# Optimization experiments

Measured on AMD Instinct MI355X. Metric: run time of the kernel, lower is better.

The kernel has to match this reference:

```python
import jax, jax.numpy as jnp
import numpy as np

NUM_HEAD = 8
HIDDEN = 1024


def setup_inputs() -> dict:
    key = jax.random.key(0)
    ks = jax.random.split(key, 7)
    B, Q, K = 2, 256, 256
    return {
        "query": jax.random.normal(ks[0], (B, Q, HIDDEN), jnp.float32),
        "keys": jax.random.normal(ks[1], (B, K, HIDDEN), jnp.float32),
        "values": jax.random.normal(ks[2], (B, K, HIDDEN), jnp.float32),
        "mask": jax.random.randint(ks[3], (B, K), 0, 2, jnp.int32),
        "W_q": jax.random.normal(ks[4], (HIDDEN, HIDDEN), jnp.float32),
        "W_k": jax.random.normal(ks[5], (HIDDEN, HIDDEN), jnp.float32),
        "V_a": jax.random.normal(ks[6], (HIDDEN,), jnp.float32),
    }


def reference(query, keys, values, mask, W_q, W_k, V_a):
    B, Q, H = query.shape
    K = keys.shape[1]
    h_q = query @ W_q                                   # [B,Q,H]
    h_k = keys @ W_k                                    # [B,K,H]
    # additive (Bahdanau) scores, split hidden into heads and sum per head
    h = jnp.tanh(h_q[:, :, None, :] + h_k[:, None, :, :]) * V_a   # [B,Q,K,H]
    logits = h.reshape(B, Q, K, NUM_HEAD, H // NUM_HEAD).sum(-1)  # [B,Q,K,h]
    logits = jnp.transpose(logits, (0, 3, 1, 2))        # [B,h,Q,K]
    penalty = (1.0 - mask.astype(jnp.float32)) * 99.0   # [B,K]
    logits = logits - penalty[:, None, None, :]
    weights = jax.nn.softmax(logits, axis=-1)           # [B,h,Q,K]
    v = values.reshape(B, K, NUM_HEAD, H // NUM_HEAD)   # [B,K,h,d]
    ctx = jnp.einsum('bhqk,bkhd->bqhd', weights, v).reshape(B, Q, H)
    return ctx, weights
```

## Files before the change

### kernel.cpp

```cpp
#include <hip/hip_runtime.h>
#include <hip/hip_bf16.h>


#define TANH_SCALE 2.88539008177792681472f
#define LOG2E      1.44269504088896340736f

typedef __attribute__((ext_vector_type(8))) short bf16x8_t;
typedef __attribute__((ext_vector_type(4))) float f32x4_t;

__device__ inline ushort bf16_rne(float f) {
  unsigned u = __float_as_uint(f);
  u += 0x7FFFu + ((u >> 16) & 1u);
  return (ushort)(u >> 16);
}
__device__ inline float bf16_to_f(ushort h) { return __uint_as_float((unsigned)h << 16); }
__device__ inline void split1(float v, ushort& hi, ushort& lo) {
  hi = bf16_rne(v);
  lo = bf16_rne(v - bf16_to_f(hi));
}

__global__ __launch_bounds__(256) void prep(
    const float* __restrict__ query, const float* __restrict__ keys,
    const float* __restrict__ Wq, const float* __restrict__ Wk,
    ushort* __restrict__ qhi, ushort* __restrict__ qlo,
    ushort* __restrict__ khi, ushort* __restrict__ klo,
    ushort* __restrict__ wqthi, ushort* __restrict__ wqtlo,
    ushort* __restrict__ wkthi, ushort* __restrict__ wktlo)
{
  __shared__ float t[64][65];
  const int bid = blockIdx.x, tid = threadIdx.x;
  if (bid < 1024) {
    const int z = bid >> 9;
    const float* in = z ? keys : query;
    ushort* hi = z ? khi : qhi;
    ushort* lo = z ? klo : qlo;
    const size_t i = ((size_t)(bid & 511) * 256 + tid) * 4;
    float4 v = *(const float4*)(in + i);
    ushort h0, h1, h2, h3, l0, l1, l2, l3;
    split1(v.x, h0, l0); split1(v.y, h1, l1);
    split1(v.z, h2, l2); split1(v.w, h3, l3);
    *(ushort4*)(hi + i) = make_ushort4(h0, h1, h2, h3);
    *(ushort4*)(lo + i) = make_ushort4(l0, l1, l2, l3);
  } else {
    const int idx = bid - 1024;
    const int z = idx >> 8;
    const float* W = z ? Wk : Wq;
    ushort* thi = z ? wkthi : wqthi;
    ushort* tlo = z ? wktlo : wqtlo;
    const int n0 = (idx & 15) * 64, h0 = ((idx >> 4) & 15) * 64;
    const int r = tid >> 4, c = (tid & 15) * 4;
#pragma unroll
    for (int i = 0; i < 4; ++i) {
      const int rr = r + i * 16;
      float4 wv = *(const float4*)(W + (size_t)(h0 + rr) * 1024 + n0 + c);
      t[rr][c + 0] = wv.x; t[rr][c + 1] = wv.y;
      t[rr][c + 2] = wv.z; t[rr][c + 3] = wv.w;
    }
    __syncthreads();
#pragma unroll
    for (int i = 0; i < 4; ++i) {
      const int rr = r + i * 16;
      ushort h0v, h1v, h2v, h3v, l0v, l1v, l2v, l3v;
      split1(t[c + 0][rr] * TANH_SCALE, h0v, l0v);
      split1(t[c + 1][rr] * TANH_SCALE, h1v, l1v);
      split1(t[c + 2][rr] * TANH_SCALE, h2v, l2v);
      split1(t[c + 3][rr] * TANH_SCALE, h3v, l3v);
      *(ushort4*)(thi + (size_t)(n0 + rr) * 1024 + h0 + c) = make_ushort4(h0v, h1v, h2v, h3v);
      *(ushort4*)(tlo + (size_t)(n0 + rr) * 1024 + h0 + c) = make_ushort4(l0v, l1v, l2v, l3v);
    }
  }
}

__global__ __launch_bounds__(256) void gemm_mfma(
    const ushort* __restrict__ qhi, const ushort* __restrict__ qlo,
    const ushort* __restrict__ khi, const ushort* __restrict__ klo,
    const ushort* __restrict__ wqthi, const ushort* __restrict__ wqtlo,
    const ushort* __restrict__ wkthi, const ushort* __restrict__ wktlo,
    float* __restrict__ GQ, float* __restrict__ GKT)
{
  const int z = blockIdx.y;
  const int bid = blockIdx.x;
  int m0, n0, ldc;
  const ushort *Ah_g, *Al_g, *Bh_g, *Bl_g;
  float* Gp;
  if (z == 0) {
    m0 = (bid >> 4) * 64; n0 = (bid & 15) * 64; ldc = 1024;
    Ah_g = qhi; Al_g = qlo; Bh_g = wqthi; Bl_g = wqtlo; Gp = GQ;
  } else {
    m0 = (bid >> 3) * 64; n0 = (bid & 7) * 64; ldc = 512;
    Ah_g = wkthi; Al_g = wktlo; Bh_g = khi; Bl_g = klo; Gp = GKT;
  }

  __shared__ __align__(16) ushort Ah[64 * 40];
  __shared__ __align__(16) ushort Al[64 * 40];
  __shared__ __align__(16) ushort Bh[64 * 40];
  __shared__ __align__(16) ushort Bl[64 * 40];

  const int tid = threadIdx.x;
  const int srow = tid >> 2, skc = (tid & 3) * 8;
  const size_t gA = (size_t)(m0 + srow) * 1024 + skc;
  const size_t gB = (size_t)(n0 + srow) * 1024 + skc;
  const int soff = srow * 40 + skc;

  uint4 rah = *(const uint4*)(Ah_g + gA);
  uint4 ral = *(const uint4*)(Al_g + gA);
  uint4 rbh = *(const uint4*)(Bh_g + gB);
  uint4 rbl = *(const uint4*)(Bl_g + gB);

  const int w = __builtin_amdgcn_readfirstlane(tid >> 6);
  const int lane = tid & 63;
  const int wm = (w >> 1) * 32, wn = (w & 1) * 32;
  const int fr = lane & 15, kg = lane >> 4;
  const int aoff = (wm + fr) * 40 + kg * 8;
  const int boff = (wn + fr) * 40 + kg * 8;

  f32x4_t acc[2][2] = {};

  for (int kk = 0; kk < 1024; kk += 32) {
    __syncthreads();
    *(uint4*)(Ah + soff) = rah;
    *(uint4*)(Al + soff) = ral;
    *(uint4*)(Bh + soff) = rbh;
    *(uint4*)(Bl + soff) = rbl;
    __syncthreads();

    if (kk + 32 < 1024) {
      rah = *(const uint4*)(Ah_g + gA + kk + 32);
      ral = *(const uint4*)(Al_g + gA + kk + 32);
      rbh = *(const uint4*)(Bh_g + gB + kk + 32);
      rbl = *(const uint4*)(Bl_g + gB + kk + 32);
    }

    bf16x8_t ah0 = *(const bf16x8_t*)(Ah + aoff);
    bf16x8_t ah1 = *(const bf16x8_t*)(Ah + aoff + 16 * 40);
    bf16x8_t al0 = *(const bf16x8_t*)(Al + aoff);
    bf16x8_t al1 = *(const bf16x8_t*)(Al + aoff + 16 * 40);
    bf16x8_t bh0 = *(const bf16x8_t*)(Bh + boff);
    bf16x8_t bh1 = *(const bf16x8_t*)(Bh + boff + 16 * 40);
    bf16x8_t bl0 = *(const bf16x8_t*)(Bl + boff);
    bf16x8_t bl1 = *(const bf16x8_t*)(Bl + boff + 16 * 40);

    acc[0][0] = __builtin_amdgcn_mfma_f32_16x16x32_bf16(ah0, bh0, acc[0][0], 0, 0, 0);
    acc[0][1] = __builtin_amdgcn_mfma_f32_16x16x32_bf16(ah0, bh1, acc[0][1], 0, 0, 0);
    acc[1][0] = __builtin_amdgcn_mfma_f32_16x16x32_bf16(ah1, bh0, acc[1][0], 0, 0, 0);
    acc[1][1] = __builtin_amdgcn_mfma_f32_16x16x32_bf16(ah1, bh1, acc[1][1], 0, 0, 0);
    acc[0][0] = __builtin_amdgcn_mfma_f32_16x16x32_bf16(ah0, bl0, acc[0][0], 0, 0, 0);
    acc[0][1] = __builtin_amdgcn_mfma_f32_16x16x32_bf16(ah0, bl1, acc[0][1], 0, 0, 0);
    acc[1][0] = __builtin_amdgcn_mfma_f32_16x16x32_bf16(ah1, bl0, acc[1][0], 0, 0, 0);
    acc[1][1] = __builtin_amdgcn_mfma_f32_16x16x32_bf16(ah1, bl1, acc[1][1], 0, 0, 0);
    acc[0][0] = __builtin_amdgcn_mfma_f32_16x16x32_bf16(al0, bh0, acc[0][0], 0, 0, 0);
    acc[0][1] = __builtin_amdgcn_mfma_f32_16x16x32_bf16(al0, bh1, acc[0][1], 0, 0, 0);
    acc[1][0] = __builtin_amdgcn_mfma_f32_16x16x32_bf16(al1, bh0, acc[1][0], 0, 0, 0);
    acc[1][1] = __builtin_amdgcn_mfma_f32_16x16x32_bf16(al1, bh1, acc[1][1], 0, 0, 0);
  }

#pragma unroll
  for (int fm = 0; fm < 2; ++fm)
#pragma unroll
    for (int fn = 0; fn < 2; ++fn) {
      const int col = n0 + wn + fn * 16 + fr;
#pragma unroll
      for (int j = 0; j < 4; ++j) {
        const int row = m0 + wm + fm * 16 + kg * 4 + j;
        Gp[(size_t)row * ldc + col] = __builtin_amdgcn_exp2f(acc[fm][fn][j] * 0.125f);
      }
    }
}

__global__ __launch_bounds__(256) void attn_fused(
    const float* __restrict__ GQ, const float* __restrict__ GKT,
    const float* __restrict__ Va, const int* __restrict__ mask,
    const float* __restrict__ values,
    float* __restrict__ weights, float* __restrict__ ctx)
{
  __shared__ __align__(16) float gq_s[8][128];
  __shared__ __align__(16) float va_s[128];
  __shared__ float red_m[4][8];
  __shared__ float red_s[4][8];
  __shared__ __align__(16) float P_lds[8][256];

  const int tid = threadIdx.x;
  const int lane = tid & 63;
  const int w = __builtin_amdgcn_readfirstlane(tid >> 6);
  const int bid = blockIdx.x;
  const int bh = bid >> 5;
  const int b = bh & 1, h = bh >> 1;
  const int qt = (bid & 31) * 8;
  const int k = w * 64 + lane;

  {
    const int sq = tid >> 5, sd = (tid & 31) * 4;
    *(float4*)&gq_s[sq][sd] =
        *(const float4*)(GQ + (size_t)(b * 256 + qt + sq) * 1024 + h * 128 + sd);
    if (tid < 32) *(float4*)&va_s[tid * 4] = *(const float4*)(Va + h * 128 + tid * 4);
  }

  const float pen = 99.0f * (1.0f - (float)mask[b * 256 + k]);

  float ssum = Va[h * 128 + lane] + Va[h * 128 + 64 + lane];
#pragma unroll
  for (int off = 32; off; off >>= 1) ssum += __shfl_xor(ssum, off, 64);

  const float* gkp = GKT + (size_t)(h * 128) * 512 + b * 256 + k;

  __syncthreads();

  float acc0[8] = {0.f, 0.f, 0.f, 0.f, 0.f, 0.f, 0.f, 0.f};
  float acc1[8] = {0.f, 0.f, 0.f, 0.f, 0.f, 0.f, 0.f, 0.f};

  float gkc[8];
#pragma unroll
  for (int j = 0; j < 8; ++j) gkc[j] = gkp[(size_t)j * 512];

  for (int ch = 0; ch < 16; ++ch) {
    const int d0 = ch * 8;
    float gkn[8];
    if (ch < 15) {
#pragma unroll
      for (int j = 0; j < 8; ++j) gkn[j] = gkp[(size_t)(d0 + 8 + j) * 512];
    }
    float var_[8];
    *(float4*)&var_[0] = *(const float4*)&va_s[d0];
    *(float4*)&var_[4] = *(const float4*)&va_s[d0 + 4];
#pragma unroll
    for (int q = 0; q < 8; ++q) {
      float gqr[8];
      *(float4*)&gqr[0] = *(const float4*)&gq_s[q][d0];
      *(float4*)&gqr[4] = *(const float4*)&gq_s[q][d0 + 4];
#pragma unroll
      for (int e = 0; e < 8; ++e) {
        const float u  = gqr[e] * gkc[e];
        const float u2 = u * u;
        const float u4 = u2 * u2;
        const float t  = u4 * u4;
        const float r  = __builtin_amdgcn_rcpf(t + 1.0f);
        if (e & 1) acc1[q] += var_[e] * r; else acc0[q] += var_[e] * r;
      }
    }
    if (ch < 15) {
#pragma unroll
      for (int j = 0; j < 8; ++j) gkc[j] = gkn[j];
    }
  }

  float l[8], p[8];
#pragma unroll
  for (int q = 0; q < 8; ++q) l[q] = ssum - 2.0f * (acc0[q] + acc1[q]) - pen;

#pragma unroll
  for (int q = 0; q < 8; ++q) {
    float m = l[q];
#pragma unroll
    for (int off = 32; off; off >>= 1) m = fmaxf(m, __shfl_xor(m, off, 64));
    if (lane == 0) red_m[w][q] = m;
  }
  __syncthreads();
#pragma unroll
  for (int q = 0; q < 8; ++q) {
    float m = fmaxf(fmaxf(red_m[0][q], red_m[1][q]), fmaxf(red_m[2][q], red_m[3][q]));
    p[q] = __builtin_amdgcn_exp2f((l[q] - m) * LOG2E);
  }
#pragma unroll
  for (int q = 0; q < 8; ++q) {
    float s = p[q];
#pragma unroll
    for (int off = 32; off; off >>= 1) s += __shfl_xor(s, off, 64);
    if (lane == 0) red_s[w][q] = s;
  }
  __syncthreads();
#pragma unroll
  for (int q = 0; q < 8; ++q) {
    const float s = (red_s[0][q] + red_s[1][q]) + (red_s[2][q] + red_s[3][q]);
    const float pq = p[q] / s;
    weights[((size_t)((b * 8 + h) * 256) + qt + q) * 256 + k] = pq;
    P_lds[q][k] = pq;
  }
  __syncthreads();

  const int d4 = lane & 31, ks = lane >> 5;
  const int q0 = w * 2, q1 = q0 + 1;
  const float* vb = values + (size_t)(b * 256 + ks * 128) * 1024 + h * 128 + d4 * 4;
  float4 A0 = make_float4(0, 0, 0, 0), A1 = make_float4(0, 0, 0, 0);
#pragma unroll 2
  for (int k4 = 0; k4 < 32; ++k4) {
    float4 p0v = *(const float4*)&P_lds[q0][ks * 128 + k4 * 4];
    float4 p1v = *(const float4*)&P_lds[q1][ks * 128 + k4 * 4];
#pragma unroll
    for (int j = 0; j < 4; ++j) {
      float4 v = *(const float4*)(vb + (size_t)(k4 * 4 + j) * 1024);
      const float pj0 = (j == 0) ? p0v.x : (j == 1) ? p0v.y : (j == 2) ? p0v.z : p0v.w;
      const float pj1 = (j == 0) ? p1v.x : (j == 1) ? p1v.y : (j == 2) ? p1v.z : p1v.w;
      A0.x += pj0 * v.x; A0.y += pj0 * v.y; A0.z += pj0 * v.z; A0.w += pj0 * v.w;
      A1.x += pj1 * v.x; A1.y += pj1 * v.y; A1.z += pj1 * v.z; A1.w += pj1 * v.w;
    }
  }
  A0.x += __shfl_xor(A0.x, 32, 64); A0.y += __shfl_xor(A0.y, 32, 64);
  A0.z += __shfl_xor(A0.z, 32, 64); A0.w += __shfl_xor(A0.w, 32, 64);
  A1.x += __shfl_xor(A1.x, 32, 64); A1.y += __shfl_xor(A1.y, 32, 64);
  A1.z += __shfl_xor(A1.z, 32, 64); A1.w += __shfl_xor(A1.w, 32, 64);
  if (lane < 32) {
    *(float4*)&ctx[(size_t)(b * 256 + qt + q0) * 1024 + h * 128 + d4 * 4] = A0;
    *(float4*)&ctx[(size_t)(b * 256 + qt + q1) * 1024 + h * 128 + d4 * 4] = A1;
  }
}

extern "C" void kernel_launch(void* const* d_in, const int* in_sizes, int n_in,
                              void* d_out, int out_size, void* d_ws, size_t ws_size,
                              hipStream_t stream) {
  const float* query  = (const float*)d_in[0];
  const float* keys   = (const float*)d_in[1];
  const float* values = (const float*)d_in[2];
  const int*   mask   = (const int*)d_in[3];
  const float* Wq     = (const float*)d_in[4];
  const float* Wk     = (const float*)d_in[5];
  const float* Va     = (const float*)d_in[6];

  float* ctx     = (float*)d_out;
  float* weights = ctx + 524288;

  ushort* qhi   = (ushort*)d_ws;
  ushort* qlo   = qhi + 524288;
  ushort* khi   = qlo + 524288;
  ushort* klo   = khi + 524288;
  ushort* wqthi = klo + 524288;
  ushort* wqtlo = wqthi + 1048576;
  ushort* wkthi = wqtlo + 1048576;
  ushort* wktlo = wkthi + 1048576;
  float*  GQ    = (float*)(wktlo + 1048576);
  float*  GKT   = GQ + 524288;

  prep<<<dim3(1536), 256, 0, stream>>>(query, keys, Wq, Wk,
                                       qhi, qlo, khi, klo,
                                       wqthi, wqtlo, wkthi, wktlo);
  gemm_mfma<<<dim3(128, 2), 256, 0, stream>>>(qhi, qlo, khi, klo,
                                              wqthi, wqtlo, wkthi, wktlo, GQ, GKT);
  attn_fused<<<dim3(512), 256, 0, stream>>>(GQ, GKT, Va, mask, values, weights, ctx);
}
```

Measured before the change: 67.15 us.

## Split attention hidden dim across 8 waves and batch reciprocals per four terms

Launches the fused attention kernel with 512 threads and splits the per-head hidden dimension across two wave groups, combining partial score sums and the P·V partials through LDS. The inner tanh-as-rational loop merges four 1/(1+t) terms into one fraction, so it needs a single rcp instead of four, with a clamp on u so the eighth power cannot overflow. The intent is fewer transcendental ops and more waves per block to hide latency. The cost is extra LDS traffic and barriers, and some added rounding risk from the combined rational form.

```diff
diff --git a/kernel.cpp b/kernel.cpp
--- a/kernel.cpp
+++ b/kernel.cpp
@@ -4,6 +4,7 @@
 
 #define TANH_SCALE 2.88539008177792681472f
 #define LOG2E      1.44269504088896340736f
+#define UCLAMP     13.0f
 
 typedef __attribute__((ext_vector_type(8))) short bf16x8_t;
 typedef __attribute__((ext_vector_type(4))) float f32x4_t;
@@ -17,6 +18,12 @@
 __device__ inline void split1(float v, ushort& hi, ushort& lo) {
   hi = bf16_rne(v);
   lo = bf16_rne(v - bf16_to_f(hi));
+}
+__device__ inline float pow8c(float u) {
+  u = fminf(u, UCLAMP);
+  float u2 = u * u;
+  float u4 = u2 * u2;
+  return u4 * u4;
 }
 
 __global__ __launch_bounds__(256) void prep(
@@ -167,7 +174,7 @@
     }
 }
 
-__global__ __launch_bounds__(256) void attn_fused(
+__global__ __launch_bounds__(512) void attn_fused(
     const float* __restrict__ GQ, const float* __restrict__ GKT,
     const float* __restrict__ Va, const int* __restrict__ mask,
     const float* __restrict__ values,
@@ -175,9 +182,11 @@
 {
   __shared__ __align__(16) float gq_s[8][128];
   __shared__ __align__(16) float va_s[128];
+  __shared__ __align__(16) float acc_lds[4][64][8];
   __shared__ float red_m[4][8];
   __shared__ float red_s[4][8];
   __shared__ __align__(16) float P_lds[8][256];
+  __shared__ __align__(16) float4 pv_part[4][2][32];
 
   const int tid = threadIdx.x;
   const int lane = tid & 63;
@@ -186,12 +195,14 @@
   const int bh = bid >> 5;
   const int b = bh & 1, h = bh >> 1;
   const int qt = (bid & 31) * 8;
-  const int k = w * 64 + lane;
+  const int dh = w >> 2, kq = w & 3;
+  const int k = kq * 64 + lane;
 
   {
-    const int sq = tid >> 5, sd = (tid & 31) * 4;
-    *(float4*)&gq_s[sq][sd] =
-        *(const float4*)(GQ + (size_t)(b * 256 + qt + sq) * 1024 + h * 128 + sd);
+    const int i2 = tid * 2;
+    const int sq = i2 >> 7, sd = i2 & 127;
+    *(float2*)&gq_s[sq][sd] =
+        *(const float2*)(GQ + (size_t)(b * 256 + qt + sq) * 1024 + h * 128 + sd);
     if (tid < 32) *(float4*)&va_s[tid * 4] = *(const float4*)(Va + h * 128 + tid * 4);
   }
 
@@ -201,106 +212,146 @@
 #pragma unroll
   for (int off = 32; off; off >>= 1) ssum += __shfl_xor(ssum, off, 64);
 
-  const float* gkp = GKT + (size_t)(h * 128) * 512 + b * 256 + k;
-
-  __syncthreads();
-
-  float acc0[8] = {0.f, 0.f, 0.f, 0.f, 0.f, 0.f, 0.f, 0.f};
-  float acc1[8] = {0.f, 0.f, 0.f, 0.f, 0.f, 0.f, 0.f, 0.f};
+  const float* gkp = GKT + (size_t)(h * 128 + dh * 64) * 512 + b * 256 + k;
+
+  __syncthreads();
+
+  float acc[8] = {0.f, 0.f, 0.f, 0.f, 0.f, 0.f, 0.f, 0.f};
 
   float gkc[8];
 #pragma unroll
   for (int j = 0; j < 8; ++j) gkc[j] = gkp[(size_t)j * 512];
 
-  for (int ch = 0; ch < 16; ++ch) {
+  for (int ch = 0; ch < 8; ++ch) {
     const int d0 = ch * 8;
     float gkn[8];
-    if (ch < 15) {
+    if (ch < 7) {
 #pragma unroll
       for (int j = 0; j < 8; ++j) gkn[j] = gkp[(size_t)(d0 + 8 + j) * 512];
     }
-    float var_[8];
-    *(float4*)&var_[0] = *(const float4*)&va_s[d0];
-    *(float4*)&var_[4] = *(const float4*)&va_s[d0 + 4];
+    float va_[8];
+    *(float4*)&va_[0] = *(const float4*)&va_s[dh * 64 + d0];
+    *(float4*)&va_[4] = *(const float4*)&va_s[dh * 64 + d0 + 4];
+    const float s01 = va_[0] + va_[1], s23 = va_[2] + va_[3];
+    const float s45 = va_[4] + va_[5], s67 = va_[6] + va_[7];
 #pragma unroll
     for (int q = 0; q < 8; ++q) {
       float gqr[8];
-      *(float4*)&gqr[0] = *(const float4*)&gq_s[q][d0];
-      *(float4*)&gqr[4] = *(const float4*)&gq_s[q][d0 + 4];
-#pragma unroll
-      for (int e = 0; e < 8; ++e) {
-        const float u  = gqr[e] * gkc[e];
-        const float u2 = u * u;
-        const float u4 = u2 * u2;
-        const float t  = u4 * u4;
-        const float r  = __builtin_amdgcn_rcpf(t + 1.0f);
-        if (e & 1) acc1[q] += var_[e] * r; else acc0[q] += var_[e] * r;
+      *(float4*)&gqr[0] = *(const float4*)&gq_s[q][dh * 64 + d0];
+      *(float4*)&gqr[4] = *(const float4*)&gq_s[q][dh * 64 + d0 + 4];
+      {
+        const float t0 = pow8c(gqr[0] * gkc[0]);
+        const float t1 = pow8c(gqr[1] * gkc[1]);
+        const float t2 = pow8c(gqr[2] * gkc[2]);
+        const float t3 = pow8c(gqr[3] * gkc[3]);
+        const float p01 = fmaf(t0, t1, t0 + t1 + 1.0f);
+        const float p23 = fmaf(t2, t3, t2 + t3 + 1.0f);
+        const float den = p01 * p23;
+        const float n01 = fmaf(va_[0], t1, fmaf(va_[1], t0, s01));
+        const float n23 = fmaf(va_[2], t3, fmaf(va_[3], t2, s23));
+        const float N = fmaf(n01, p23, n23 * p01);
+        acc[q] = fmaf(N, __builtin_amdgcn_rcpf(den), acc[q]);
       }
-    }
-    if (ch < 15) {
+      {
+        const float t0 = pow8c(gqr[4] * gkc[4]);
+        const float t1 = pow8c(gqr[5] * gkc[5]);
+        const float t2 = pow8c(gqr[6] * gkc[6]);
+        const float t3 = pow8c(gqr[7] * gkc[7]);
+        const float p01 = fmaf(t0, t1, t0 + t1 + 1.0f);
+        const float p23 = fmaf(t2, t3, t2 + t3 + 1.0f);
+        const float den = p01 * p23;
+        const float n01 = fmaf(va_[4], t1, fmaf(va_[5], t0, s45));
+        const float n23 = fmaf(va_[6], t3, fmaf(va_[7], t2, s67));
+        const float N = fmaf(n01, p23, n23 * p01);
+        acc[q] = fmaf(N, __builtin_amdgcn_rcpf(den), acc[q]);
+      }
+    }
+    if (ch < 7) {
 #pragma unroll
       for (int j = 0; j < 8; ++j) gkc[j] = gkn[j];
     }
   }
 
+  if (w >= 4) {
+#pragma unroll
+    for (int q = 0; q < 8; ++q) acc_lds[kq][lane][q] = acc[q];
+  }
+  __syncthreads();
+
   float l[8], p[8];
-#pragma unroll
-  for (int q = 0; q < 8; ++q) l[q] = ssum - 2.0f * (acc0[q] + acc1[q]) - pen;
-
-#pragma unroll
-  for (int q = 0; q < 8; ++q) {
-    float m = l[q];
-#pragma unroll
-    for (int off = 32; off; off >>= 1) m = fmaxf(m, __shfl_xor(m, off, 64));
-    if (lane == 0) red_m[w][q] = m;
-  }
-  __syncthreads();
-#pragma unroll
-  for (int q = 0; q < 8; ++q) {
-    float m = fmaxf(fmaxf(red_m[0][q], red_m[1][q]), fmaxf(red_m[2][q], red_m[3][q]));
-    p[q] = __builtin_amdgcn_exp2f((l[q] - m) * LOG2E);
-  }
-#pragma unroll
-  for (int q = 0; q < 8; ++q) {
-    float s = p[q];
-#pragma unroll
-    for (int off = 32; off; off >>= 1) s += __shfl_xor(s, off, 64);
-    if (lane == 0) red_s[w][q] = s;
-  }
-  __syncthreads();
-#pragma unroll
-  for (int q = 0; q < 8; ++q) {
-    const float s = (red_s[0][q] + red_s[1][q]) + (red_s[2][q] + red_s[3][q]);
-    const float pq = p[q] / s;
-    weights[((size_t)((b * 8 + h) * 256) + qt + q) * 256 + k] = pq;
-    P_lds[q][k] = pq;
-  }
-  __syncthreads();
-
-  const int d4 = lane & 31, ks = lane >> 5;
-  const int q0 = w * 2, q1 = q0 + 1;
-  const float* vb = values + (size_t)(b * 256 + ks * 128) * 1024 + h * 128 + d4 * 4;
-  float4 A0 = make_float4(0, 0, 0, 0), A1 = make_float4(0, 0, 0, 0);
-#pragma unroll 2
-  for (int k4 = 0; k4 < 32; ++k4) {
-    float4 p0v = *(const float4*)&P_lds[q0][ks * 128 + k4 * 4];
-    float4 p1v = *(const float4*)&P_lds[q1][ks * 128 + k4 * 4];
-#pragma unroll
-    for (int j = 0; j < 4; ++j) {
-      float4 v = *(const float4*)(vb + (size_t)(k4 * 4 + j) * 1024);
-      const float pj0 = (j == 0) ? p0v.x : (j == 1) ? p0v.y : (j == 2) ? p0v.z : p0v.w;
-      const float pj1 = (j == 0) ? p1v.x : (j == 1) ? p1v.y : (j == 2) ? p1v.z : p1v.w;
-      A0.x += pj0 * v.x; A0.y += pj0 * v.y; A0.z += pj0 * v.z; A0.w += pj0 * v.w;
-      A1.x += pj1 * v.x; A1.y += pj1 * v.y; A1.z += pj1 * v.z; A1.w += pj1 * v.w;
-    }
-  }
-  A0.x += __shfl_xor(A0.x, 32, 64); A0.y += __shfl_xor(A0.y, 32, 64);
-  A0.z += __shfl_xor(A0.z, 32, 64); A0.w += __shfl_xor(A0.w, 32, 64);
-  A1.x += __shfl_xor(A1.x, 32, 64); A1.y += __shfl_xor(A1.y, 32, 64);
-  A1.z += __shfl_xor(A1.z, 32, 64); A1.w += __shfl_xor(A1.w, 32, 64);
-  if (lane < 32) {
-    *(float4*)&ctx[(size_t)(b * 256 + qt + q0) * 1024 + h * 128 + d4 * 4] = A0;
-    *(float4*)&ctx[(size_t)(b * 256 + qt + q1) * 1024 + h * 128 + d4 * 4] = A1;
+  if (w < 4) {
+#pragma unroll
+    for (int q = 0; q < 8; ++q) {
+      acc[q] += acc_lds[kq][lane][q];
+      l[q] = ssum - 2.0f * acc[q] - pen;
+    }
+#pragma unroll
+    for (int q = 0; q < 8; ++q) {
+      float m = l[q];
+#pragma unroll
+      for (int off = 32; off; off >>= 1) m = fmaxf(m, __shfl_xor(m, off, 64));
+      if (lane == 0) red_m[w][q] = m;
+    }
+  }
+  __syncthreads();
+  if (w < 4) {
+#pragma unroll
+    for (int q = 0; q < 8; ++q) {
+      float m = fmaxf(fmaxf(red_m[0][q], red_m[1][q]), fmaxf(red_m[2][q], red_m[3][q]));
+      p[q] = __builtin_amdgcn_exp2f((l[q] - m) * LOG2E);
+    }
+#pragma unroll
+    for (int q = 0; q < 8; ++q) {
+      float s = p[q];
+#pragma unroll
+      for (int off = 32; off; off >>= 1) s += __shfl_xor(s, off, 64);
+      if (lane == 0) red_s[w][q] = s;
+    }
+  }
+  __syncthreads();
+  if (w < 4) {
+#pragma unroll
+    for (int q = 0; q < 8; ++q) {
+      const float s = (red_s[0][q] + red_s[1][q]) + (red_s[2][q] + red_s[3][q]);
+      const float pq = p[q] / s;
+      weights[((size_t)((b * 8 + h) * 256) + qt + q) * 256 + k] = pq;
+      P_lds[q][k] = pq;
+    }
+  }
+  __syncthreads();
+
+  {
+    const int rp = w & 3, kh = w >> 2;
+    const int d4 = lane & 31, ks = lane >> 5;
+    const int q0 = rp * 2, q1 = q0 + 1;
+    const float* vb = values + (size_t)(b * 256 + kh * 128 + ks * 64) * 1024 + h * 128 + d4 * 4;
+    const float* w0p = &P_lds[q0][kh * 128 + ks * 64];
+    const float* w1p = &P_lds[q1][kh * 128 + ks * 64];
+    float4 A0 = make_float4(0, 0, 0, 0), A1 = make_float4(0, 0, 0, 0);
+#pragma unroll 4
+    for (int j = 0; j < 64; ++j) {
+      float4 v = *(const float4*)(vb + (size_t)j * 1024);
+      const float pw0 = w0p[j], pw1 = w1p[j];
+      A0.x += pw0 * v.x; A0.y += pw0 * v.y; A0.z += pw0 * v.z; A0.w += pw0 * v.w;
+      A1.x += pw1 * v.x; A1.y += pw1 * v.y; A1.z += pw1 * v.z; A1.w += pw1 * v.w;
+    }
+    A0.x += __shfl_xor(A0.x, 32, 64); A0.y += __shfl_xor(A0.y, 32, 64);
+    A0.z += __shfl_xor(A0.z, 32, 64); A0.w += __shfl_xor(A0.w, 32, 64);
+    A1.x += __shfl_xor(A1.x, 32, 64); A1.y += __shfl_xor(A1.y, 32, 64);
+    A1.z += __shfl_xor(A1.z, 32, 64); A1.w += __shfl_xor(A1.w, 32, 64);
+    if (w >= 4 && lane < 32) {
+      pv_part[rp][0][d4] = A0;
+      pv_part[rp][1][d4] = A1;
+    }
+    __syncthreads();
+    if (w < 4 && lane < 32) {
+      float4 pa = pv_part[rp][0][d4];
+      float4 pb = pv_part[rp][1][d4];
+      A0.x += pa.x; A0.y += pa.y; A0.z += pa.z; A0.w += pa.w;
+      A1.x += pb.x; A1.y += pb.y; A1.z += pb.z; A1.w += pb.w;
+      *(float4*)&ctx[(size_t)(b * 256 + qt + q0) * 1024 + h * 128 + d4 * 4] = A0;
+      *(float4*)&ctx[(size_t)(b * 256 + qt + q1) * 1024 + h * 128 + d4 * 4] = A1;
+    }
   }
 }
 
@@ -334,5 +385,5 @@
                                        wqthi, wqtlo, wkthi, wktlo);
   gemm_mfma<<<dim3(128, 2), 256, 0, stream>>>(qhi, qlo, khi, klo,
                                               wqthi, wqtlo, wkthi, wktlo, GQ, GKT);
-  attn_fused<<<dim3(512), 256, 0, stream>>>(GQ, GKT, Va, mask, values, weights, ctx);
-}
+  attn_fused<<<dim3(512), 512, 0, stream>>>(GQ, GKT, Va, mask, values, weights, ctx);
+}
```

Result: no change. 66.28 us (-1.3%).
